# Optimization experiments

Hardware: AMD Instinct MI355X
Metric: run time of the kernel (lower is better)

Reference implementation:

```python
import jax, jax.numpy as jnp
import numpy as np

N_NODES = 100000
N_EDGES = 1600000
N_FEAT = 128
HIDDEN = 128
N_CLASSES = 10
N_GRAPHS = 64


def setup_inputs() -> dict:
    key = jax.random.key(0)
    ks = jax.random.split(key, 9)
    x = jax.random.normal(ks[0], (N_NODES, N_FEAT), dtype=jnp.float32)
    edge_index = jax.random.randint(ks[1], (2, N_EDGES), 0, N_NODES, dtype=jnp.int64)
    batch = jnp.sort(jax.random.randint(ks[2], (N_NODES,), 0, N_GRAPHS, dtype=jnp.int64))
    # GCNConv weights (stored as [in, out] for x @ W) and biases
    s1 = 1.0 / np.sqrt(N_FEAT)
    s2 = 1.0 / np.sqrt(HIDDEN)
    W1 = jax.random.uniform(ks[3], (N_FEAT, HIDDEN), jnp.float32, -s1, s1)
    b1 = jnp.zeros((HIDDEN,), jnp.float32)
    W2 = jax.random.uniform(ks[4], (HIDDEN, HIDDEN), jnp.float32, -s2, s2)
    b2 = jnp.zeros((HIDDEN,), jnp.float32)
    Wfc = jax.random.uniform(ks[5], (HIDDEN, N_CLASSES), jnp.float32, -s2, s2)
    bfc = jax.random.uniform(ks[6], (N_CLASSES,), jnp.float32, -s2, s2)
    return {"x": x, "edge_index": edge_index, "batch": batch,
            "W1": W1, "b1": b1, "W2": W2, "b2": b2, "Wfc": Wfc, "bfc": bfc}


def gcn_conv(x, W, b, src, dst, n_nodes):
    # PyG GCNConv: add self-loops, symmetric normalization D^-1/2 A D^-1/2,
    # linear transform, scatter-add aggregation, plus bias.
    h = x @ W  # [N, H]
    deg = jax.ops.segment_sum(jnp.ones_like(dst, dtype=x.dtype), dst,
                              num_segments=n_nodes)  # in-degree incl. self loops
    dis = jnp.where(deg > 0, jax.lax.rsqrt(deg), 0.0)
    norm = dis[src] * dis[dst]  # [E+N]
    msg = h[src] * norm[:, None]  # gather + scale
    out = jax.ops.segment_sum(msg, dst, num_segments=n_nodes)  # scatter-add
    return out + b


def reference(x, edge_index, batch, W1, b1, W2, b2, Wfc, bfc):
    n = x.shape[0]
    loops = jnp.arange(n, dtype=edge_index.dtype)
    src = jnp.concatenate([edge_index[0], loops])
    dst = jnp.concatenate([edge_index[1], loops])

    h = jax.nn.relu(gcn_conv(x, W1, b1, src, dst, n))
    h = jax.nn.relu(gcn_conv(h, W2, b2, src, dst, n))

    # global_mean_pool over graph ids
    sums = jax.ops.segment_sum(h, batch, num_segments=N_GRAPHS)  # [B, H]
    cnts = jax.ops.segment_sum(jnp.ones((n,), h.dtype), batch,
                               num_segments=N_GRAPHS)
    pooled = sums / jnp.maximum(cnts, 1.0)[:, None]
    return pooled @ Wfc + bfc  # [B, C]
```

## Files before the change

### kernel.cpp

```cpp
#include <hip/hip_runtime.h>
#include <hip/hip_bf16.h>


typedef __attribute__((ext_vector_type(8))) short s16x8;
typedef __attribute__((ext_vector_type(4))) float f32x4;

#define BSH 9
#define BNODES 512
#define SRC_BITS 17
#define SRC_MASK ((1u << SRC_BITS) - 1u)
#define EPB 4096

__device__ inline float bflo(unsigned int u) { return __uint_as_float(u << 16); }
__device__ inline float bfhi(unsigned int u) { return __uint_as_float(u & 0xFFFF0000u); }
__device__ inline unsigned short f2bf(float f) {
    unsigned int u = __float_as_uint(f);
    unsigned int r = (u + 0x7FFFu + ((u >> 16) & 1u)) >> 16;
    return (unsigned short)r;
}
__device__ inline unsigned int packbf2(float a, float b) {
    return (unsigned int)f2bf(a) | ((unsigned int)f2bf(b) << 16);
}

__global__ __launch_bounds__(512) void bucket_scatter_kernel(const int* __restrict__ src, const int* __restrict__ dst,
                                                             int E, int cap, int* __restrict__ gfill,
                                                             unsigned int* __restrict__ gbuf, int nsc,
                                                             const float* __restrict__ W1, const float* __restrict__ W2,
                                                             short* __restrict__ WT1, short* __restrict__ WT2,
                                                             short* __restrict__ bufA, int n) {
    __shared__ int hist[256];
    __shared__ int loff[256];
    __shared__ int basea[256];
    __shared__ int rk[256];
    __shared__ int wsum[4];
    __shared__ unsigned int sorted[EPB];
    __shared__ unsigned char bko[EPB];
    int t = threadIdx.x;
    if ((int)blockIdx.x >= nsc) {
        int g = ((int)blockIdx.x - nsc) * 512 + t;
        const float* W = (g < 16384) ? W1 : W2;
        short* WT = (g < 16384) ? WT1 : WT2;
        int tt = g & 16383;
        int k = tt >> 7, nn = tt & 127;
        WT[nn * 128 + k] = f2bf(W[tt]);
        if ((int)blockIdx.x == nsc && t < 64) ((unsigned int*)(bufA + (size_t)n * 128))[t] = 0u;
        return;
    }
    if (t < 256) { hist[t] = 0; rk[t] = 0; }
    __syncthreads();
    int e0 = blockIdx.x * EPB;
    unsigned int wreg[EPB / 512];
    int breg[EPB / 512];
    #pragma unroll
    for (int i = 0; i < EPB / 512; i++) {
        int e = e0 + i * 512 + t;
        if (e < E) {
            int d = dst[e], s = src[e];
            int b = d >> BSH;
            wreg[i] = ((unsigned int)(d & (BNODES - 1)) << SRC_BITS) | (unsigned int)s;
            breg[i] = b;
            atomicAdd(&hist[b], 1);
        } else breg[i] = -1;
    }
    __syncthreads();
    int h = 0, incl = 0;
    if (t < 256) {
        h = hist[t];
        incl = h;
        int lane = t & 63;
        #pragma unroll
        for (int d = 1; d < 64; d <<= 1) {
            int u = __shfl_up(incl, d);
            if (lane >= d) incl += u;
        }
        if (lane == 63) wsum[t >> 6] = incl;
    }
    __syncthreads();
    if (t < 256) {
        int w = t >> 6;
        int wbase = 0;
        #pragma unroll
        for (int i = 0; i < 4; i++) if (i < w) wbase += wsum[i];
        loff[t] = wbase + incl - h;
        basea[t] = (h > 0) ? atomicAdd(&gfill[t], h) : 0;
    }
    __syncthreads();
    #pragma unroll
    for (int i = 0; i < EPB / 512; i++) {
        int b = breg[i];
        if (b >= 0) {
            int slot = loff[b] + atomicAdd(&rk[b], 1);
            sorted[slot] = wreg[i];
            bko[slot] = (unsigned char)b;
        }
    }
    __syncthreads();
    int ntot = loff[255] + hist[255];
    for (int i = t; i < ntot; i += 512) {
        int b = bko[i];
        int pos = basea[b] + (i - loff[b]);
        if (pos < cap) gbuf[(size_t)b * cap + pos] = sorted[i];
    }
}

__global__ __launch_bounds__(1024) void bucket_countfill_kernel(const unsigned int* __restrict__ gbuf,
                                                                const int* __restrict__ gfill, int cap, int n,
                                                                int* __restrict__ cnt, int* __restrict__ offA,
                                                                float* __restrict__ dis, int* __restrict__ g_total,
                                                                int* __restrict__ csr) {
    int b = blockIdx.x, t = threadIdx.x;
    int d0 = b << BSH;
    __shared__ int cl[BNODES];
    __shared__ int wsum[4];
    __shared__ int gbase_s;
    if (t < BNODES) cl[t] = 0;
    __syncthreads();
    int ne = min(gfill[b], cap);
    const unsigned int* eb = gbuf + (size_t)b * cap;
    for (int i = t; i < ne; i += 1024) atomicAdd(&cl[eb[i] >> SRC_BITS], 1);
    __syncthreads();
    int v0 = 0, v1 = 0, p0 = 0, p1 = 0, incl = 0, s = 0;
    if (t < 256) {
        v0 = cl[2 * t]; v1 = cl[2 * t + 1];
        p0 = (v0 + 7) & ~7; p1 = (v1 + 7) & ~7;
        s = p0 + p1;
        incl = s;
        int lane = t & 63;
        #pragma unroll
        for (int dd = 1; dd < 64; dd <<= 1) {
            int u = __shfl_up(incl, dd);
            if (lane >= dd) incl += u;
        }
        if (lane == 63) wsum[t >> 6] = incl;
    }
    __syncthreads();
    if (t == 0) gbase_s = atomicAdd(g_total, wsum[0] + wsum[1] + wsum[2] + wsum[3]);
    __syncthreads();
    int o0 = 0, o1 = 0;
    if (t < 256) {
        int w = t >> 6;
        int wbase = 0;
        #pragma unroll
        for (int i = 0; i < 4; i++) if (i < w) wbase += wsum[i];
        int excl = wbase + incl - s;
        int gbase = gbase_s;
        o0 = gbase + excl; o1 = o0 + p0;
        int i0 = d0 + 2 * t, i1 = i0 + 1;
        if (i0 < n) { cnt[i0] = p0; offA[i0] = o0; dis[i0] = rsqrtf((float)(v0 + 1)); }
        if (i1 < n) { cnt[i1] = p1; offA[i1] = o1; dis[i1] = rsqrtf((float)(v1 + 1)); }
        cl[2 * t] = o0; cl[2 * t + 1] = o1;
    }
    __syncthreads();
    for (int i = t; i < ne; i += 1024) {
        unsigned int wd = eb[i];
        int li = wd >> SRC_BITS;
        int slot = atomicAdd(&cl[li], 1);
        csr[slot] = (int)(wd & SRC_MASK);
    }
    __syncthreads();
    if (t < 256) {
        for (int j = o0 + v0; j < o0 + p0; j++) csr[j] = n;
        for (int j = o1 + v1; j < o1 + p1; j++) csr[j] = n;
    }
}

template <bool F32IN>
__global__ __launch_bounds__(256) void gemm_mfma_kernel(const void* __restrict__ Xv, const short* __restrict__ WTb,
                                                        const float* __restrict__ dis,
                                                        short* __restrict__ Yb, int n, int ntiles) {
    int lane = threadIdx.x & 63;
    int m = lane & 15, kg = lane >> 4;
    int gwave = (int)((blockIdx.x * 256 + threadIdx.x) >> 6);
    if (gwave >= ntiles) return;

    s16x8 bfr[8][4];
    #pragma unroll
    for (int t = 0; t < 8; t++)
        #pragma unroll
        for (int ks = 0; ks < 4; ks++)
            bfr[t][ks] = *(const s16x8*)(WTb + ((m * 8 + t) * 128 + ks * 32 + kg * 8));

    int rbase = gwave * 16;
    int row = rbase + m;
    size_t rc = (size_t)(row < n ? row : n - 1);
    s16x8 afr[4];
    if constexpr (F32IN) {
        const float* xrow = (const float*)Xv + rc * 128 + kg * 8;
        #pragma unroll
        for (int ks = 0; ks < 4; ks++) {
            float4 a0 = *(const float4*)(xrow + ks * 32);
            float4 a1 = *(const float4*)(xrow + ks * 32 + 4);
            s16x8 f;
            f[0] = (short)f2bf(a0.x); f[1] = (short)f2bf(a0.y);
            f[2] = (short)f2bf(a0.z); f[3] = (short)f2bf(a0.w);
            f[4] = (short)f2bf(a1.x); f[5] = (short)f2bf(a1.y);
            f[6] = (short)f2bf(a1.z); f[7] = (short)f2bf(a1.w);
            afr[ks] = f;
        }
    } else {
        const short* xrow = (const short*)Xv + rc * 128 + kg * 8;
        #pragma unroll
        for (int ks = 0; ks < 4; ks++) afr[ks] = *(const s16x8*)(xrow + ks * 32);
    }
    f32x4 acc[8];
    #pragma unroll
    for (int t = 0; t < 8; t++) acc[t] = (f32x4)(0.f);
    #pragma unroll
    for (int ks = 0; ks < 4; ks++)
        #pragma unroll
        for (int t = 0; t < 8; t++)
            acc[t] = __builtin_amdgcn_mfma_f32_16x16x32_bf16(afr[ks], bfr[t][ks], acc[t], 0, 0, 0);
    int orow0 = rbase + kg * 4;
    #pragma unroll
    for (int r = 0; r < 4; r++) {
        int orow = orow0 + r;
        if (orow < n) {
            float dv = dis[orow];
            s16x8 y;
            #pragma unroll
            for (int t = 0; t < 8; t++) y[t] = (short)f2bf(acc[t][r] * dv);
            *(s16x8*)(Yb + (size_t)orow * 128 + m * 8) = y;
        }
    }
}

__global__ __launch_bounds__(256) void agg_kernel(const short* __restrict__ H, const int* __restrict__ csr,
                                                  const int* __restrict__ offA, const int* __restrict__ cnt,
                                                  const float* __restrict__ dis, const float* __restrict__ bias,
                                                  short* __restrict__ O, int n) {
    int wid = __builtin_amdgcn_readfirstlane((int)((blockIdx.x * 256 + threadIdx.x) >> 6));
    int lane = threadIdx.x & 63;
    int half = lane >> 5, fl = lane & 31;
    if (wid >= n) return;
    int base = __builtin_amdgcn_readfirstlane(offA[wid]);
    int c = __builtin_amdgcn_readfirstlane(cnt[wid]);
    float d = dis[wid];
    float a0 = 0.f, a1 = 0.f, a2 = 0.f, a3 = 0.f;
    if (half == 0) {
        uint2 sv = ((const uint2*)(H + (size_t)wid * 128))[fl];
        a0 = bflo(sv.x); a1 = bfhi(sv.x);
        a2 = bflo(sv.y); a3 = bfhi(sv.y);
    }
    for (int k = 0; k < c; k += 8) {
        int4 q0 = *(const int4*)(csr + base + k);
        int4 q1 = *(const int4*)(csr + base + k + 4);
        int r0 = half ? q0.y : q0.x;
        int r1 = half ? q0.w : q0.z;
        int r2 = half ? q1.y : q1.x;
        int r3 = half ? q1.w : q1.z;
        uint2 h0 = ((const uint2*)(H + (size_t)r0 * 128))[fl];
        uint2 h1 = ((const uint2*)(H + (size_t)r1 * 128))[fl];
        uint2 h2 = ((const uint2*)(H + (size_t)r2 * 128))[fl];
        uint2 h3 = ((const uint2*)(H + (size_t)r3 * 128))[fl];
        a0 += bflo(h0.x); a1 += bfhi(h0.x); a2 += bflo(h0.y); a3 += bfhi(h0.y);
        a0 += bflo(h1.x); a1 += bfhi(h1.x); a2 += bflo(h1.y); a3 += bfhi(h1.y);
        a0 += bflo(h2.x); a1 += bfhi(h2.x); a2 += bflo(h2.y); a3 += bfhi(h2.y);
        a0 += bflo(h3.x); a1 += bfhi(h3.x); a2 += bflo(h3.y); a3 += bfhi(h3.y);
    }
    a0 += __shfl_xor(a0, 32);
    a1 += __shfl_xor(a1, 32);
    a2 += __shfl_xor(a2, 32);
    a3 += __shfl_xor(a3, 32);
    if (half == 0) {
        float4 b = ((const float4*)bias)[fl];
        float o0 = a0 * d + b.x, o1 = a1 * d + b.y;
        float o2 = a2 * d + b.z, o3 = a3 * d + b.w;
        o0 = fmaxf(o0, 0.f); o1 = fmaxf(o1, 0.f);
        o2 = fmaxf(o2, 0.f); o3 = fmaxf(o3, 0.f);
        ((uint2*)(O + (size_t)wid * 128))[fl] = make_uint2(packbf2(o0, o1), packbf2(o2, o3));
    }
}

__global__ __launch_bounds__(1024) void poolfc_kernel(const short* __restrict__ H, const int* __restrict__ batch,
                                                      const float* __restrict__ Wfc, const float* __restrict__ bfc,
                                                      float* __restrict__ out, int n) {
    int g = blockIdx.x;
    int t = threadIdx.x;
    int w = t >> 6, lane = t & 63;
    int lo = 0, hi = n;
    while (lo < hi) { int mid = (lo + hi) >> 1; if (batch[mid] < g) lo = mid + 1; else hi = mid; }
    int lo2 = lo; hi = n;
    while (lo2 < hi) { int mid = (lo2 + hi) >> 1; if (batch[mid] < g + 1) lo2 = mid + 1; else hi = mid; }
    float ax = 0.f, ay = 0.f;
    for (int i = lo + w; i < lo2; i += 16) {
        unsigned int u = ((const unsigned int*)(H + (size_t)i * 128))[lane];
        ax += bflo(u); ay += bfhi(u);
    }
    __shared__ float red[16][128];
    red[w][2 * lane] = ax;
    red[w][2 * lane + 1] = ay;
    __syncthreads();
    __shared__ float pv[128];
    if (w == 0) {
        float s0 = 0.f, s1 = 0.f;
        #pragma unroll
        for (int r = 0; r < 16; r++) { s0 += red[r][2 * lane]; s1 += red[r][2 * lane + 1]; }
        float inv = 1.0f / fmaxf((float)(lo2 - lo), 1.0f);
        pv[2 * lane] = s0 * inv;
        pv[2 * lane + 1] = s1 * inv;
    }
    __syncthreads();
    if (t < 10) {
        float acc = 0.f;
        for (int k = 0; k < 128; k++) acc += pv[k] * Wfc[k * 10 + t];
        out[g * 10 + t] = acc + bfc[t];
    }
}

extern "C" void kernel_launch(void* const* d_in, const int* in_sizes, int n_in,
                              void* d_out, int out_size, void* d_ws, size_t ws_size,
                              hipStream_t stream) {
    const float* x   = (const float*)d_in[0];
    const int*   ei  = (const int*)d_in[1];
    const int*   bat = (const int*)d_in[2];
    const float* W1  = (const float*)d_in[3];
    const float* b1  = (const float*)d_in[4];
    const float* W2  = (const float*)d_in[5];
    const float* b2  = (const float*)d_in[6];
    const float* Wfc = (const float*)d_in[7];
    const float* bfc = (const float*)d_in[8];
    int n = in_sizes[0] / 128;
    int E = in_sizes[1] / 2;
    const int* src = ei;
    const int* dst = ei + E;

    int nbuck = (n + BNODES - 1) >> BSH;
    int cap = ((E / nbuck) * 2 + 512 + 63) & ~63;

    char* ws = (char*)d_ws;
    size_t off = 0;
    auto alloc = [&](size_t bytes) -> void* {
        void* p = ws + off;
        off = (off + bytes + 511) & ~(size_t)511;
        return p;
    };
    int*   gfill  = (int*)alloc(256 * 4);
    int*   gtotal = (int*)alloc(512);
    size_t zero_bytes = off;
    int*   cnt   = (int*)alloc((size_t)n * 4);
    int*   offA  = (int*)alloc((size_t)n * 4);
    float* dis   = (float*)alloc((size_t)n * 4);
    unsigned int* gbuf = (unsigned int*)alloc((size_t)nbuck * cap * 4);
    int*   csr   = (int*)alloc(((size_t)E + 8 * (size_t)(n + 1)) * 4);
    short* wt1   = (short*)alloc(128 * 128 * 2);
    short* wt2   = (short*)alloc(128 * 128 * 2);
    short* bufA  = (short*)alloc((size_t)(n + 1) * 128 * 2);
    short* bufB  = (short*)alloc((size_t)(n + 1) * 128 * 2);
    (void)ws_size;

    int ntiles = (n + 15) / 16;
    int gemm_blocks = (ntiles + 3) / 4;
    int nsc = (E + EPB - 1) / EPB;

    hipMemsetAsync(d_ws, 0, zero_bytes, stream);
    bucket_scatter_kernel<<<nsc + 64, 512, 0, stream>>>(src, dst, E, cap, gfill, gbuf, nsc,
                                                        W1, W2, wt1, wt2, bufA, n);
    bucket_countfill_kernel<<<nbuck, 1024, 0, stream>>>(gbuf, gfill, cap, n, cnt, offA, dis, gtotal, csr);

    gemm_mfma_kernel<true><<<gemm_blocks, 256, 0, stream>>>(x, wt1, dis, bufA, n, ntiles);
    agg_kernel<<<((size_t)n * 64 + 255) / 256, 256, 0, stream>>>(bufA, csr, offA, cnt, dis, b1, bufB, n);
    gemm_mfma_kernel<false><<<gemm_blocks, 256, 0, stream>>>(bufB, wt2, dis, bufA, n, ntiles);
    agg_kernel<<<((size_t)n * 64 + 255) / 256, 256, 0, stream>>>(bufA, csr, offA, cnt, dis, b2, bufB, n);

    poolfc_kernel<<<64, 1024, 0, stream>>>(bufB, bat, Wfc, bfc, (float*)d_out, n);
}
```

Measured before the change: 351.9 us.

## Sort CSR neighbors by source partition and vectorize pooling loads

The count/fill kernel now keeps per-node counters split into eight source-index partitions, so each node's CSR neighbor list comes out grouped by source range. This should improve locality of the later feature gathers in the aggregation kernels. The pooling kernel switches to 16-byte loads covering four rows per wave, reduced with shuffles. The cost is eight times more shared-memory counters and an extra prefix pass per node.

Result: faster. 332.8 us (-5.4%).

```diff
diff --git a/kernel.cpp b/kernel.cpp
--- a/kernel.cpp
+++ b/kernel.cpp
@@ -10,6 +10,8 @@
 #define SRC_BITS 17
 #define SRC_MASK ((1u << SRC_BITS) - 1u)
 #define EPB 4096
+#define NPART 8
+#define PSH 14
 
 __device__ inline float bflo(unsigned int u) { return __uint_as_float(u << 16); }
 __device__ inline float bfhi(unsigned int u) { return __uint_as_float(u & 0xFFFF0000u); }
@@ -110,18 +112,27 @@
                                                                 int* __restrict__ csr) {
     int b = blockIdx.x, t = threadIdx.x;
     int d0 = b << BSH;
-    __shared__ int cl[BNODES];
+    __shared__ int cl2[BNODES * NPART];
+    __shared__ int nodeoff[BNODES];
     __shared__ int wsum[4];
     __shared__ int gbase_s;
-    if (t < BNODES) cl[t] = 0;
+    for (int i = t; i < BNODES * NPART; i += 1024) cl2[i] = 0;
     __syncthreads();
     int ne = min(gfill[b], cap);
     const unsigned int* eb = gbuf + (size_t)b * cap;
-    for (int i = t; i < ne; i += 1024) atomicAdd(&cl[eb[i] >> SRC_BITS], 1);
+    for (int i = t; i < ne; i += 1024) {
+        unsigned int wd = eb[i];
+        int li = wd >> SRC_BITS;
+        int part = (int)((wd & SRC_MASK) >> PSH);
+        atomicAdd(&cl2[li * NPART + part], 1);
+    }
     __syncthreads();
     int v0 = 0, v1 = 0, p0 = 0, p1 = 0, incl = 0, s = 0;
     if (t < 256) {
-        v0 = cl[2 * t]; v1 = cl[2 * t + 1];
+        #pragma unroll
+        for (int j = 0; j < NPART; j++) v0 += cl2[(2 * t) * NPART + j];
+        #pragma unroll
+        for (int j = 0; j < NPART; j++) v1 += cl2[(2 * t + 1) * NPART + j];
         p0 = (v0 + 7) & ~7; p1 = (v1 + 7) & ~7;
         s = p0 + p1;
         incl = s;
@@ -136,7 +147,6 @@
     __syncthreads();
     if (t == 0) gbase_s = atomicAdd(g_total, wsum[0] + wsum[1] + wsum[2] + wsum[3]);
     __syncthreads();
-    int o0 = 0, o1 = 0;
     if (t < 256) {
         int w = t >> 6;
         int wbase = 0;
@@ -144,23 +154,36 @@
         for (int i = 0; i < 4; i++) if (i < w) wbase += wsum[i];
         int excl = wbase + incl - s;
         int gbase = gbase_s;
-        o0 = gbase + excl; o1 = o0 + p0;
+        int o0 = gbase + excl, o1 = o0 + p0;
         int i0 = d0 + 2 * t, i1 = i0 + 1;
         if (i0 < n) { cnt[i0] = p0; offA[i0] = o0; dis[i0] = rsqrtf((float)(v0 + 1)); }
         if (i1 < n) { cnt[i1] = p1; offA[i1] = o1; dis[i1] = rsqrtf((float)(v1 + 1)); }
-        cl[2 * t] = o0; cl[2 * t + 1] = o1;
+        nodeoff[2 * t] = o0; nodeoff[2 * t + 1] = o1;
+    }
+    __syncthreads();
+    if (t < BNODES) {
+        int run = nodeoff[t];
+        #pragma unroll
+        for (int j = 0; j < NPART; j++) {
+            int c = cl2[t * NPART + j];
+            cl2[t * NPART + j] = run;
+            run += c;
+        }
     }
     __syncthreads();
     for (int i = t; i < ne; i += 1024) {
         unsigned int wd = eb[i];
         int li = wd >> SRC_BITS;
-        int slot = atomicAdd(&cl[li], 1);
+        int part = (int)((wd & SRC_MASK) >> PSH);
+        int slot = atomicAdd(&cl2[li * NPART + part], 1);
         csr[slot] = (int)(wd & SRC_MASK);
     }
     __syncthreads();
-    if (t < 256) {
-        for (int j = o0 + v0; j < o0 + p0; j++) csr[j] = n;
-        for (int j = o1 + v1; j < o1 + p1; j++) csr[j] = n;
+    if (t < BNODES) {
+        int base = nodeoff[t];
+        int end = cl2[t * NPART + NPART - 1];
+        int p = ((end - base) + 7) & ~7;
+        for (int j = end; j < base + p; j++) csr[j] = n;
     }
 }
 
@@ -277,18 +300,31 @@
     int g = blockIdx.x;
     int t = threadIdx.x;
     int w = t >> 6, lane = t & 63;
+    int q = lane >> 4, fl4 = lane & 15;
     int lo = 0, hi = n;
     while (lo < hi) { int mid = (lo + hi) >> 1; if (batch[mid] < g) lo = mid + 1; else hi = mid; }
     int lo2 = lo; hi = n;
     while (lo2 < hi) { int mid = (lo2 + hi) >> 1; if (batch[mid] < g + 1) lo2 = mid + 1; else hi = mid; }
-    float ax = 0.f, ay = 0.f;
-    for (int i = lo + w; i < lo2; i += 16) {
-        unsigned int u = ((const unsigned int*)(H + (size_t)i * 128))[lane];
-        ax += bflo(u); ay += bfhi(u);
+    float ac[8];
+    #pragma unroll
+    for (int j = 0; j < 8; j++) ac[j] = 0.f;
+    for (int i = lo + w * 4 + q; i < lo2; i += 64) {
+        uint4 u = ((const uint4*)(H + (size_t)i * 128))[fl4];
+        ac[0] += bflo(u.x); ac[1] += bfhi(u.x);
+        ac[2] += bflo(u.y); ac[3] += bfhi(u.y);
+        ac[4] += bflo(u.z); ac[5] += bfhi(u.z);
+        ac[6] += bflo(u.w); ac[7] += bfhi(u.w);
+    }
+    #pragma unroll
+    for (int j = 0; j < 8; j++) {
+        ac[j] += __shfl_xor(ac[j], 16);
+        ac[j] += __shfl_xor(ac[j], 32);
     }
     __shared__ float red[16][128];
-    red[w][2 * lane] = ax;
-    red[w][2 * lane + 1] = ay;
+    if (lane < 16) {
+        #pragma unroll
+        for (int j = 0; j < 8; j++) red[w][fl4 * 8 + j] = ac[j];
+    }
     __syncthreads();
     __shared__ float pv[128];
     if (w == 0) {
```
